# Performance work log

Measured on AMD Instinct MI355X. Metric: run time of the kernel, lower is better.

Reference implementation:

```python
import jax, jax.numpy as jnp
import numpy as np
from jax import lax

NC = 8  # num_classes
NUM_ITERS = 2


def _resize_bilinear_ac(x, out_h, out_w):
    """Bilinear resize with align_corners=True, x: (N, C, H, W)."""
    N, C, H, W = x.shape

    def coords(n_out, n_in):
        if n_out == 1:
            return jnp.zeros((1,), jnp.float32)
        return jnp.linspace(0.0, float(n_in - 1), n_out, dtype=jnp.float32)

    ys = coords(out_h, H)
    xs = coords(out_w, W)
    y0 = jnp.floor(ys).astype(jnp.int32)
    y1 = jnp.minimum(y0 + 1, H - 1)
    wy = (ys - y0.astype(jnp.float32)).astype(x.dtype)
    x0 = jnp.floor(xs).astype(jnp.int32)
    x1 = jnp.minimum(x0 + 1, W - 1)
    wx = (xs - x0.astype(jnp.float32)).astype(x.dtype)

    r0 = x[:, :, y0, :]
    r1 = x[:, :, y1, :]
    r = r0 * (1.0 - wy)[None, None, :, None] + r1 * wy[None, None, :, None]
    c0 = r[:, :, :, x0]
    c1 = r[:, :, :, x1]
    return c0 * (1.0 - wx)[None, None, None, :] + c1 * wx[None, None, None, :]


def _conv2d(x, w, groups=1):
    k = w.shape[-1]
    pad = k // 2
    return lax.conv_general_dilated(
        x, w, window_strides=(1, 1), padding=[(pad, pad), (pad, pad)],
        dimension_numbers=('NCHW', 'OIHW', 'NCHW'), feature_group_count=groups)


def _mean_field_update(unary, guidance, spatial_w, bilateral_w, compat_w):
    Q = jax.nn.softmax(unary, axis=1)
    cw = compat_w[:, :, 0, 0]  # (O, I)
    for _ in range(NUM_ITERS):
        spatial_msg = _conv2d(Q, spatial_w, groups=NC)          # depthwise 3x3
        bilateral_in = jnp.concatenate([Q, guidance], axis=1)   # (N, NC+6, H, W)
        bilateral_msg = _conv2d(bilateral_in, bilateral_w)      # 3x3 dense
        message = spatial_msg + bilateral_msg
        message = jnp.einsum('nchw,oc->nohw', message, cw)      # 1x1 compat conv
        Q = jax.nn.softmax(unary - message, axis=1)
    return Q


def setup_inputs() -> dict:
    key = jax.random.key(0)
    ks = jax.random.split(key, 16)
    inp = {
        'logits': jax.random.normal(ks[0], (8, NC, 512, 512), jnp.float32),
        'image': jax.random.uniform(ks[1], (8, 3, 512, 512), jnp.float32),
        'skip0': jax.random.normal(ks[2], (8, 64, 256, 256), jnp.float32),
        'skip1': jax.random.normal(ks[3], (8, 128, 128, 128), jnp.float32),
        'skip2': jax.random.normal(ks[4], (8, 256, 64, 64), jnp.float32),
        'skip3': jax.random.normal(ks[5], (8, 512, 32, 32), jnp.float32),
        'spatial_w': jax.random.normal(ks[6], (NC, 1, 3, 3), jnp.float32) * 0.1,
        'bilateral_w': jax.random.normal(ks[7], (NC, NC + 6, 3, 3), jnp.float32) * 0.1,
        # compat_conv is initialized to -I (zeros then -= eye) in the module
        'compat_w': (-jnp.eye(NC, dtype=jnp.float32)).reshape(NC, NC, 1, 1),
        'skip_w0': jax.random.normal(ks[8], (3, 64, 1, 1), jnp.float32) * 0.05,
        'skip_b0': jnp.zeros((3,), jnp.float32),
        'skip_w1': jax.random.normal(ks[9], (3, 128, 1, 1), jnp.float32) * 0.05,
        'skip_b1': jnp.zeros((3,), jnp.float32),
        'skip_w2': jax.random.normal(ks[10], (3, 256, 1, 1), jnp.float32) * 0.05,
        'skip_b2': jnp.zeros((3,), jnp.float32),
        'skip_w3': jax.random.normal(ks[11], (3, 512, 1, 1), jnp.float32) * 0.05,
        'skip_b3': jnp.zeros((3,), jnp.float32),
    }
    return inp


def reference(logits, image, skip0, skip1, skip2, skip3,
              spatial_w, bilateral_w, compat_w,
              skip_w0, skip_b0, skip_w1, skip_b1,
              skip_w2, skip_b2, skip_w3, skip_b3):
    H, W = logits.shape[2], logits.shape[3]

    # fuse_skip_features: 1x1 project each skip to 3ch, upsample, average
    skips = [skip0, skip1, skip2, skip3]
    ws = [skip_w0, skip_w1, skip_w2, skip_w3]
    bs = [skip_b0, skip_b1, skip_b2, skip_b3]
    fused = jnp.zeros((logits.shape[0], 3, H, W), logits.dtype)
    for feat, w, b in zip(skips, ws, bs):
        p = jnp.einsum('nchw,oc->nohw', feat, w[:, :, 0, 0]) + b[None, :, None, None]
        fused = fused + _resize_bilinear_ac(p, H, W)
    fused = fused / len(skips)

    guidance = jnp.concatenate([image, fused], axis=1)  # (N, 6, H, W)

    Q_full = _mean_field_update(logits, guidance, spatial_w, bilateral_w, compat_w)

    logits_down = _resize_bilinear_ac(logits, H // 2, W // 2)
    guidance_down = _resize_bilinear_ac(guidance, H // 2, W // 2)
    Q_down = _mean_field_update(logits_down, guidance_down, spatial_w, bilateral_w, compat_w)
    Q_down_up = _resize_bilinear_ac(Q_down, H, W)

    return (Q_full + Q_down_up) / 2.0
```

## Files before the change

### kernel.cpp

```cpp
#include <hip/hip_runtime.h>
#include <hip/hip_fp16.h>
#include <math.h>

#define NB 8
#define NCLS 8
#define NGU 6
#define NBI 14
#define HF 512
#define WF 512
#define HH 256
#define WH 256

#define TOX 32
#define TOY 16
#define SX 36
#define SY 20
#define SPX (SY * SX)
#define R1W 36
#define R1N (18 * 36)
#define R1T 41
#define R2T 32
#define PLANE (SPX * 8)
#define PSTR (PLANE + 32)
#define TILEH (16 + PSTR + PLANE + 16)

typedef _Float16 f16x8 __attribute__((ext_vector_type(8)));
typedef float f32x4 __attribute__((ext_vector_type(4)));

static __device__ __forceinline__ void ac_prep(int o, float scale, int insz,
                                               int& i0, int& i1, float& f) {
    float s = (float)o * scale;
    int ii = (int)floorf(s);
    if (ii > insz - 1) ii = insz - 1;
    if (ii < 0) ii = 0;
    i0 = ii;
    i1 = (ii + 1 < insz) ? (ii + 1) : (insz - 1);
    f = s - (float)ii;
}

static __device__ __forceinline__ void dma16(const _Float16* g, _Float16* l) {
    __builtin_amdgcn_global_load_lds(
        (const __attribute__((address_space(1))) void*)g,
        (__attribute__((address_space(3))) void*)l, 16, 0, 0);
}
static __device__ __forceinline__ void dma16f(const float* g, float* l) {
    __builtin_amdgcn_global_load_lds(
        (const __attribute__((address_space(1))) void*)g,
        (__attribute__((address_space(3))) void*)l, 16, 0, 0);
}

__global__ void k_prep_wf(const float* __restrict__ wsp, const float* __restrict__ wbil,
                          const float* __restrict__ cw, _Float16* __restrict__ wf) {
    __shared__ float sW2[NBI * 72];
    int tid = threadIdx.x;
    if (tid < NBI * 72) {
        int o = tid & 7;
        int t = (tid >> 3) % 9;
        int ci = tid / 72;
        float s = 0.f;
        for (int c = 0; c < NCLS; ++c)
            s += cw[o * NCLS + c] * wbil[((size_t)c * NBI + ci) * 9 + t];
        if (ci < NCLS) s += cw[o * NCLS + ci] * wsp[ci * 9 + t];
        sW2[tid] = s;
    }
    __syncthreads();
    if (tid < 5 * 64) {
        int l = tid & 63;
        int col = l & 15, kg = l >> 4;
        #pragma unroll
        for (int e = 0; e < 8; ++e) {
            int k = (tid >> 6) * 32 + kg * 8 + e;
            int tap = k >> 4, ci = k & 15;
            float v = (tap < 9 && ci < 14 && col < 8) ? sW2[ci * 72 + tap * 8 + col] : 0.f;
            wf[tid * 8 + e] = (_Float16)v;
        }
    }
}

template <int C, int HW>
static __device__ __forceinline__ void skip_run16(
    const float* __restrict__ feat, const float* __restrict__ wg,
    const float* __restrict__ bg, float* __restrict__ out, int idx,
    float* st, float* sw, int tid, int lane, int wv) {
    for (int i = tid; i < 3 * C; i += 256) sw[i] = wg[i];
    const int pxg = idx * 256;
    const int n = pxg / HW;
    const int hw0 = pxg - n * HW;
    const float* fb = feat + (size_t)n * C * HW + hw0;
    float a0 = 0.f, a1 = 0.f, a2 = 0.f;
    for (int g = 0; g < C; g += 16) {
        #pragma unroll
        for (int r = 0; r < 4; ++r)
            dma16f(fb + (size_t)(g + wv + 4 * r) * HW + lane * 4,
                   st + (wv + 4 * r) * 256);
        __syncthreads();
        #pragma unroll
        for (int c = 0; c < 16; ++c) {
            const float v = st[c * 256 + tid];
            a0 = fmaf(sw[g + c], v, a0);
            a1 = fmaf(sw[C + g + c], v, a1);
            a2 = fmaf(sw[2 * C + g + c], v, a2);
        }
        __syncthreads();
    }
    float* op = out + (size_t)n * 3 * HW + hw0 + tid;
    op[0] = bg[0] + a0;
    op[HW] = bg[1] + a1;
    op[2 * (size_t)HW] = bg[2] + a2;
}

__global__ __launch_bounds__(256) void k_skip_all(
    const float* __restrict__ s0, const float* __restrict__ s1,
    const float* __restrict__ s2, const float* __restrict__ s3,
    const float* __restrict__ w0, const float* __restrict__ w1,
    const float* __restrict__ w2, const float* __restrict__ w3,
    const float* __restrict__ b0, const float* __restrict__ b1,
    const float* __restrict__ b2, const float* __restrict__ b3,
    float* __restrict__ p0, float* __restrict__ p1,
    float* __restrict__ p2, float* __restrict__ p3) {
    __shared__ __align__(16) float st[16 * 256];
    __shared__ float sw[3 * 512];
    const int bid = blockIdx.x;
    const int tid = threadIdx.x;
    const int lane = tid & 63;
    const int wv = tid >> 6;
    if (bid < 32)
        skip_run16<512, 1024>(s3, w3, b3, p3, bid, st, sw, tid, lane, wv);
    else if (bid < 160)
        skip_run16<256, 4096>(s2, w2, b2, p2, bid - 32, st, sw, tid, lane, wv);
    else if (bid < 672)
        skip_run16<128, 16384>(s1, w1, b1, p1, bid - 160, st, sw, tid, lane, wv);
    else
        skip_run16<64, 65536>(s0, w0, b0, p0, bid - 672, st, sw, tid, lane, wv);
}

__global__ void k_prep_full(const float* __restrict__ logits, const float* __restrict__ image,
                            const float* __restrict__ p0, const float* __restrict__ p1,
                            const float* __restrict__ p2, const float* __restrict__ p3,
                            _Float16* __restrict__ Gh, _Float16* __restrict__ Q0h) {
    const int HW = HF * WF;
    int t = blockIdx.x * blockDim.x + threadIdx.x;
    if (t >= NB * HW / 2) return;
    int idx = t * 2;
    int n = idx / HW, r = idx - n * HW;
    int y = r / WF, x = r - y * WF;

    const float* ps[4] = {p0, p1, p2, p3};
    const int ss[4] = {256, 128, 64, 32};
    float f[2][3] = {{0.f, 0.f, 0.f}, {0.f, 0.f, 0.f}};
    #pragma unroll
    for (int l = 0; l < 4; ++l) {
        int s = ss[l];
        float scale = (float)(s - 1) / 511.0f;
        int y0, y1;
        float fy;
        ac_prep(y, scale, s, y0, y1, fy);
        const float* pb = ps[l] + (size_t)n * 3 * s * s;
        #pragma unroll
        for (int k = 0; k < 2; ++k) {
            int x0, x1;
            float fx;
            ac_prep(x + k, scale, s, x0, x1, fx);
            #pragma unroll
            for (int o = 0; o < 3; ++o) {
                const float* pp = pb + (size_t)o * s * s;
                float v00 = pp[y0 * s + x0], v01 = pp[y0 * s + x1];
                float v10 = pp[y1 * s + x0], v11 = pp[y1 * s + x1];
                float r0 = v00 * (1.f - fy) + v10 * fy;
                float r1 = v01 * (1.f - fy) + v11 * fy;
                f[k][o] += r0 * (1.f - fx) + r1 * fx;
            }
        }
    }
    const float* ip = image + (size_t)n * 3 * HW + r;
    float2 img[3];
    #pragma unroll
    for (int o = 0; o < 3; ++o) img[o] = *reinterpret_cast<const float2*>(&ip[(size_t)o * HW]);
    const float* up = logits + (size_t)n * NCLS * HW + r;
    float2 u[8];
    #pragma unroll
    for (int o = 0; o < 8; ++o) u[o] = *reinterpret_cast<const float2*>(&up[(size_t)o * HW]);

    f16x8 gv[2], qv[2];
    #pragma unroll
    for (int k = 0; k < 2; ++k) {
        gv[k][0] = (_Float16)(k ? img[0].y : img[0].x);
        gv[k][1] = (_Float16)(k ? img[1].y : img[1].x);
        gv[k][2] = (_Float16)(k ? img[2].y : img[2].x);
        gv[k][3] = (_Float16)(f[k][0] * 0.25f);
        gv[k][4] = (_Float16)(f[k][1] * 0.25f);
        gv[k][5] = (_Float16)(f[k][2] * 0.25f);
        gv[k][6] = (_Float16)0.f;
        gv[k][7] = (_Float16)0.f;
        float e[8];
        float s = 0.f;
        #pragma unroll
        for (int o = 0; o < 8; ++o) { e[o] = __expf(k ? u[o].y : u[o].x); s += e[o]; }
        float inv = 1.f / s;
        #pragma unroll
        for (int o = 0; o < 8; ++o) qv[k][o] = (_Float16)(e[o] * inv);
    }
    *(f16x8*)(Gh + (size_t)idx * 8) = gv[0];
    *(f16x8*)(Gh + (size_t)idx * 8 + 8) = gv[1];
    *(f16x8*)(Q0h + (size_t)idx * 8) = qv[0];
    *(f16x8*)(Q0h + (size_t)idx * 8 + 8) = qv[1];
}

template <bool DOWN, bool UPFOLD>
__global__ __launch_bounds__(256, 4) void k_mf_mfma(
    const float* __restrict__ unary, const _Float16* __restrict__ Q0h,
    const _Float16* __restrict__ Gh, const _Float16* __restrict__ Qd,
    void* __restrict__ QoutV, const _Float16* __restrict__ wfragG,
    int H, int W, int Hs, int Ws) {
    __shared__ __align__(16) _Float16 s_t[TILEH];
    __shared__ __align__(16) _Float16 s_msg[R1N * 8];
    _Float16* tb0 = s_t + 16;
    _Float16* tb1 = s_t + 16 + PSTR;

    const int tid = threadIdx.x;
    const int lane = tid & 63;
    const int wv = tid >> 6;
    const int n = blockIdx.z;
    const int gx0 = blockIdx.x * TOX;
    const int gy0 = blockIdx.y * TOY;
    const int HW = H * W;
    const int HWs = Hs * Ws;

    f16x8 wf[5];
    #pragma unroll
    for (int j = 0; j < 5; ++j)
        wf[j] = *(const f16x8*)(wfragG + (j * 64 + lane) * 8);

    if (tid < 16) s_t[tid] = (_Float16)0.f;
    else if (tid < 48) s_t[5760 + tid] = (_Float16)0.f;
    else if (tid < 64) s_t[11520 + tid] = (_Float16)0.f;

    const bool interior = !DOWN && gx0 >= 2 && (gx0 + TOX + 2) <= W &&
                          gy0 >= 2 && (gy0 + TOY + 2) <= H;

    if (!DOWN && interior) {
        const size_t nb = (size_t)n * HW;
        for (int c = wv; c < 12; c += 4) {
            int px = c * 64 + lane;
            int yy = px / SX, xx = px - yy * SX;
            size_t goff = (nb + (size_t)(gy0 + yy - 2) * W + (gx0 + xx - 2)) * 8;
            if (px < SPX) {
                dma16(Q0h + goff, tb0 + (size_t)c * 64 * 8);
                dma16(Gh + goff, tb1 + (size_t)c * 64 * 8);
            }
        }
    } else {
        const float syc = DOWN ? (float)(Hs - 1) / (float)(H - 1) : 1.f;
        const float sxc = DOWN ? (float)(Ws - 1) / (float)(W - 1) : 1.f;
        for (int i = tid; i < SPX; i += 256) {
            int yy = i / SX, xx = i - yy * SX;
            int gy = gy0 + yy - 2, gx = gx0 + xx - 2;
            f16x8 qv, gv;
            #pragma unroll
            for (int o = 0; o < 8; ++o) { qv[o] = (_Float16)0.f; gv[o] = (_Float16)0.f; }
            if ((unsigned)gy < (unsigned)H && (unsigned)gx < (unsigned)W) {
                if (DOWN) {
                    int y0, y1, x0, x1;
                    float fy, fx;
                    ac_prep(gy, syc, Hs, y0, y1, fy);
                    ac_prep(gx, sxc, Ws, x0, x1, fx);
                    const float w00 = (1.f - fy) * (1.f - fx), w01 = (1.f - fy) * fx;
                    const float w10 = fy * (1.f - fx), w11 = fy * fx;
                    const size_t o00 = (size_t)y0 * Ws + x0, o01 = (size_t)y0 * Ws + x1;
                    const size_t o10 = (size_t)y1 * Ws + x0, o11 = (size_t)y1 * Ws + x1;
                    const float* ubase = unary + (size_t)n * NCLS * HWs;
                    float e[8];
                    float s = 0.f;
                    #pragma unroll
                    for (int o = 0; o < 8; ++o) {
                        const float* up = ubase + (size_t)o * HWs;
                        float u = w00 * up[o00] + w01 * up[o01] + w10 * up[o10] + w11 * up[o11];
                        e[o] = __expf(u);
                        s += e[o];
                    }
                    float inv = 1.f / s;
                    #pragma unroll
                    for (int o = 0; o < 8; ++o) qv[o] = (_Float16)(e[o] * inv);
                    const size_t gb = (size_t)n * HWs;
                    f16x8 ga = *(const f16x8*)(Gh + (gb + o00) * 8);
                    f16x8 gb2 = *(const f16x8*)(Gh + (gb + o01) * 8);
                    f16x8 gc = *(const f16x8*)(Gh + (gb + o10) * 8);
                    f16x8 gd = *(const f16x8*)(Gh + (gb + o11) * 8);
                    #pragma unroll
                    for (int c = 0; c < 8; ++c) {
                        float g = w00 * (float)ga[c] + w01 * (float)gb2[c] +
                                  w10 * (float)gc[c] + w11 * (float)gd[c];
                        gv[c] = (_Float16)g;
                    }
                } else {
                    const size_t off = ((size_t)n * HW + (size_t)gy * W + gx) * 8;
                    qv = *(const f16x8*)(Q0h + off);
                    gv = *(const f16x8*)(Gh + off);
                }
            }
            *(f16x8*)(tb0 + i * 8) = qv;
            *(f16x8*)(tb1 + i * 8) = gv;
        }
    }
    __syncthreads();

    for (int t = wv; t < R1T; t += 4) {
        int pb = t * 16;
        int p = pb + (lane & 15);
        if (p > R1N - 1) p = R1N - 1;
        int qy = p / R1W;
        int yy = 1 + qy, xx = p - qy * R1W;
        int kg = lane >> 4;
        f32x4 acc = {0.f, 0.f, 0.f, 0.f};
        #pragma unroll
        for (int j = 0; j < 5; ++j) {
            int tap = 2 * j + (kg >> 1);
            if (tap > 8) tap = 8;
            int dy = tap / 3 - 1, dx = tap - (tap / 3) * 3 - 1;
            int idx = (yy + dy) * SX + (xx + dx);
            f16x8 af = *(const f16x8*)(tb0 + (kg & 1) * PSTR + idx * 8);
            acc = __builtin_amdgcn_mfma_f32_16x16x32_f16(af, wf[j], acc, 0, 0, 0);
        }
        int ch = lane & 15;
        if (ch < 8) {
            int pxb = pb + (lane >> 4) * 4;
            #pragma unroll
            for (int r = 0; r < 4; ++r) {
                int px = pxb + r;
                if (px < R1N) s_msg[px * 8 + ch] = (_Float16)acc[r];
            }
        }
    }
    __syncthreads();

    for (int i = tid; i < R1N; i += 256) {
        int qy = i / R1W;
        int yy = 1 + qy, xx = i - qy * R1W;
        int gy = gy0 + yy - 2, gx = gx0 + xx - 2;
        if (interior || ((unsigned)gy < (unsigned)H && (unsigned)gx < (unsigned)W)) {
            f16x8 m = *(const f16x8*)(s_msg + i * 8);
            f16x8 q0 = *(const f16x8*)(tb0 + (i + SX) * 8);
            float e[8];
            float s = 0.f;
            #pragma unroll
            for (int o = 0; o < 8; ++o) {
                e[o] = (float)q0[o] * __expf(-(float)m[o]);
                s += e[o];
            }
            float inv = 1.f / s;
            f16x8 q1;
            #pragma unroll
            for (int o = 0; o < 8; ++o) q1[o] = (_Float16)(e[o] * inv);
            *(f16x8*)(tb0 + (i + SX) * 8) = q1;
        }
    }
    f16x8 m1r[2];
    #pragma unroll
    for (int u2 = 0; u2 < 2; ++u2) {
        int i = tid + 256 * u2;
        int oy = i >> 5, ox = i & 31;
        int r1 = (1 + oy) * R1W + (2 + ox);
        m1r[u2] = *(const f16x8*)(s_msg + r1 * 8);
    }
    __syncthreads();

    for (int t = wv; t < R2T; t += 4) {
        int pb = t * 16;
        int p = pb + (lane & 15);
        int yy = 2 + (p >> 5), xx = 2 + (p & 31);
        int kg = lane >> 4;
        f32x4 acc = {0.f, 0.f, 0.f, 0.f};
        #pragma unroll
        for (int j = 0; j < 5; ++j) {
            int tap = 2 * j + (kg >> 1);
            if (tap > 8) tap = 8;
            int dy = tap / 3 - 1, dx = tap - (tap / 3) * 3 - 1;
            int idx = (yy + dy) * SX + (xx + dx);
            f16x8 af = *(const f16x8*)(tb0 + (kg & 1) * PSTR + idx * 8);
            acc = __builtin_amdgcn_mfma_f32_16x16x32_f16(af, wf[j], acc, 0, 0, 0);
        }
        int ch = lane & 15;
        if (ch < 8) {
            int pxb = pb + (lane >> 4) * 4;
            #pragma unroll
            for (int r = 0; r < 4; ++r) s_msg[(pxb + r) * 8 + ch] = (_Float16)acc[r];
        }
    }
    __syncthreads();

    #pragma unroll
    for (int u2 = 0; u2 < 2; ++u2) {
        int i = tid + 256 * u2;
        int oy = i >> 5, ox = i & 31;
        int gy = gy0 + oy, gx = gx0 + ox;
        f16x8 m2 = *(const f16x8*)(s_msg + i * 8);
        f16x8 q1 = *(const f16x8*)(tb0 + ((2 + oy) * SX + (2 + ox)) * 8);
        float e[8];
        float s = 0.f;
        #pragma unroll
        for (int o = 0; o < 8; ++o) {
            e[o] = (float)q1[o] * __expf((float)m1r[u2][o] - (float)m2[o]);
            s += e[o];
        }
        float inv = 1.f / s;
        if (UPFOLD) {
            float* qp = (float*)QoutV + (size_t)n * NCLS * HW + (size_t)gy * W + gx;
            int y0, y1, x0, x1;
            float fy, fx;
            ac_prep(gy, 255.f / 511.f, HH, y0, y1, fy);
            ac_prep(gx, 255.f / 511.f, WH, x0, x1, fx);
            const float w00 = (1.f - fy) * (1.f - fx), w01 = (1.f - fy) * fx;
            const float w10 = fy * (1.f - fx), w11 = fy * fx;
            const size_t qb = (size_t)n * (HH * WH);
            f16x8 qa = *(const f16x8*)(Qd + (qb + (size_t)y0 * WH + x0) * 8);
            f16x8 qbv = *(const f16x8*)(Qd + (qb + (size_t)y0 * WH + x1) * 8);
            f16x8 qc = *(const f16x8*)(Qd + (qb + (size_t)y1 * WH + x0) * 8);
            f16x8 qdv = *(const f16x8*)(Qd + (qb + (size_t)y1 * WH + x1) * 8);
            #pragma unroll
            for (int o = 0; o < 8; ++o) {
                float v = w00 * (float)qa[o] + w01 * (float)qbv[o] +
                          w10 * (float)qc[o] + w11 * (float)qdv[o];
                qp[(size_t)o * HW] = fmaf(0.5f, e[o] * inv, 0.5f * v);
            }
        } else {
            _Float16* qo = (_Float16*)QoutV + ((size_t)n * HW + (size_t)gy * W + gx) * 8;
            f16x8 q2;
            #pragma unroll
            for (int o = 0; o < 8; ++o) q2[o] = (_Float16)(e[o] * inv);
            *(f16x8*)qo = q2;
        }
    }
}

static inline int cdiv(int a, int b) { return (a + b - 1) / b; }

extern "C" void kernel_launch(void* const* d_in, const int* in_sizes, int n_in,
                              void* d_out, int out_size, void* d_ws, size_t ws_size,
                              hipStream_t stream) {
    const float* logits = (const float*)d_in[0];
    const float* image = (const float*)d_in[1];
    const float* skip0 = (const float*)d_in[2];
    const float* skip1 = (const float*)d_in[3];
    const float* skip2 = (const float*)d_in[4];
    const float* skip3 = (const float*)d_in[5];
    const float* spatial_w = (const float*)d_in[6];
    const float* bilateral_w = (const float*)d_in[7];
    const float* compat_w = (const float*)d_in[8];
    const float* skip_w0 = (const float*)d_in[9];
    const float* skip_b0 = (const float*)d_in[10];
    const float* skip_w1 = (const float*)d_in[11];
    const float* skip_b1 = (const float*)d_in[12];
    const float* skip_w2 = (const float*)d_in[13];
    const float* skip_b2 = (const float*)d_in[14];
    const float* skip_w3 = (const float*)d_in[15];
    const float* skip_b3 = (const float*)d_in[16];
    float* out = (float*)d_out;
    float* ws = (float*)d_ws;

    float* p0 = ws + 0;
    float* p1 = ws + 1572864;
    float* p2 = ws + 1966080;
    float* p3 = ws + 2064384;
    _Float16* wfrag = (_Float16*)(ws + 2110000);
    _Float16* Q0h = (_Float16*)(ws + 4194304);
    _Float16* Gh = (_Float16*)(ws + 12582912);
    _Float16* Qdh = (_Float16*)(ws + 20971520);

    const int HWf = HF * WF;

    k_prep_wf<<<1, 1024, 0, stream>>>(spatial_w, bilateral_w, compat_w, wfrag);

    k_skip_all<<<2720, 256, 0, stream>>>(skip0, skip1, skip2, skip3,
                                         skip_w0, skip_w1, skip_w2, skip_w3,
                                         skip_b0, skip_b1, skip_b2, skip_b3,
                                         p0, p1, p2, p3);

    k_prep_full<<<cdiv(NB * HWf / 2, 256), 256, 0, stream>>>(
        logits, image, p0, p1, p2, p3, Gh, Q0h);

    {
        dim3 grid(WH / TOX, HH / TOY, NB);
        k_mf_mfma<true, false><<<grid, 256, 0, stream>>>(
            logits, nullptr, Gh, nullptr, (void*)Qdh, wfrag, HH, WH, HF, WF);
    }

    {
        dim3 grid(WF / TOX, HF / TOY, NB);
        k_mf_mfma<false, true><<<grid, 256, 0, stream>>>(
            nullptr, Q0h, Gh, Qdh, (void*)out, wfrag, HF, WF, HF, WF);
    }
}
```

Measured before the change: 205.9 us.

## Split skip-projection channels across threads with register loads and LDS reduction

Replaces the per-block serial channel loop, which staged 16 channels at a time into LDS via async DMA, with a kernel where each thread loads 8 channels of 4 pixels directly into registers as vector loads. Partial sums over channel slices are then reduced in shared memory. This raises the grid from 2720 to 7680 blocks to expose more memory-level parallelism on a bandwidth-bound projection over roughly 200 MB of skip features. In exchange it adds a tree reduction with several barriers and leaves most threads idle during the final store.

```diff
diff --git a/kernel.cpp b/kernel.cpp
--- a/kernel.cpp
+++ b/kernel.cpp
@@ -39,11 +39,6 @@
 }
 
 static __device__ __forceinline__ void dma16(const _Float16* g, _Float16* l) {
-    __builtin_amdgcn_global_load_lds(
-        (const __attribute__((address_space(1))) void*)g,
-        (__attribute__((address_space(3))) void*)l, 16, 0, 0);
-}
-static __device__ __forceinline__ void dma16f(const float* g, float* l) {
     __builtin_amdgcn_global_load_lds(
         (const __attribute__((address_space(1))) void*)g,
         (__attribute__((address_space(3))) void*)l, 16, 0, 0);
@@ -77,36 +72,56 @@
     }
 }
 
-template <int C, int HW>
-static __device__ __forceinline__ void skip_run16(
+template <int C, int HW, int SLICES, int PXG>
+static __device__ __forceinline__ void skip_gemm(
     const float* __restrict__ feat, const float* __restrict__ wg,
-    const float* __restrict__ bg, float* __restrict__ out, int idx,
-    float* st, float* sw, int tid, int lane, int wv) {
+    const float* __restrict__ bg, float* __restrict__ out, int bidl,
+    float* sw, f32x4* sred, int tid) {
     for (int i = tid; i < 3 * C; i += 256) sw[i] = wg[i];
-    const int pxg = idx * 256;
-    const int n = pxg / HW;
-    const int hw0 = pxg - n * HW;
-    const float* fb = feat + (size_t)n * C * HW + hw0;
-    float a0 = 0.f, a1 = 0.f, a2 = 0.f;
-    for (int g = 0; g < C; g += 16) {
-        #pragma unroll
-        for (int r = 0; r < 4; ++r)
-            dma16f(fb + (size_t)(g + wv + 4 * r) * HW + lane * 4,
-                   st + (wv + 4 * r) * 256);
+    __syncthreads();
+    const int slice = tid / PXG;
+    const int pxg = tid - slice * PXG;
+    const int pxbase = bidl * (PXG * 4);
+    const int n = pxbase / HW;
+    const int hw0 = pxbase - n * HW;
+    const float* fp = feat + ((size_t)n * C + slice * 8) * HW + hw0 + pxg * 4;
+
+    f32x4 v[8];
+    #pragma unroll
+    for (int j = 0; j < 8; ++j)
+        v[j] = *reinterpret_cast<const f32x4*>(fp + (size_t)j * HW);
+
+    f32x4 a0 = {0.f, 0.f, 0.f, 0.f};
+    f32x4 a1 = {0.f, 0.f, 0.f, 0.f};
+    f32x4 a2 = {0.f, 0.f, 0.f, 0.f};
+    #pragma unroll
+    for (int j = 0; j < 8; ++j) {
+        const int c = slice * 8 + j;
+        a0 += v[j] * sw[c];
+        a1 += v[j] * sw[C + c];
+        a2 += v[j] * sw[2 * C + c];
+    }
+    sred[0 * 256 + tid] = a0;
+    sred[1 * 256 + tid] = a1;
+    sred[2 * 256 + tid] = a2;
+    __syncthreads();
+    for (int s = 128; s > PXG; s >>= 1) {
+        if (tid < s) {
+            sred[tid] += sred[tid + s];
+            sred[256 + tid] += sred[256 + tid + s];
+            sred[512 + tid] += sred[512 + tid + s];
+        }
         __syncthreads();
-        #pragma unroll
-        for (int c = 0; c < 16; ++c) {
-            const float v = st[c * 256 + tid];
-            a0 = fmaf(sw[g + c], v, a0);
-            a1 = fmaf(sw[C + g + c], v, a1);
-            a2 = fmaf(sw[2 * C + g + c], v, a2);
-        }
-        __syncthreads();
-    }
-    float* op = out + (size_t)n * 3 * HW + hw0 + tid;
-    op[0] = bg[0] + a0;
-    op[HW] = bg[1] + a1;
-    op[2 * (size_t)HW] = bg[2] + a2;
+    }
+    if (tid < PXG) {
+        float* op = out + (size_t)n * 3 * HW + hw0 + tid * 4;
+        f32x4 r0 = sred[tid] + sred[tid + PXG] + bg[0];
+        f32x4 r1 = sred[256 + tid] + sred[256 + tid + PXG] + bg[1];
+        f32x4 r2 = sred[512 + tid] + sred[512 + tid + PXG] + bg[2];
+        *reinterpret_cast<f32x4*>(op) = r0;
+        *reinterpret_cast<f32x4*>(op + HW) = r1;
+        *reinterpret_cast<f32x4*>(op + 2 * (size_t)HW) = r2;
+    }
 }
 
 __global__ __launch_bounds__(256) void k_skip_all(
@@ -118,20 +133,18 @@
     const float* __restrict__ b2, const float* __restrict__ b3,
     float* __restrict__ p0, float* __restrict__ p1,
     float* __restrict__ p2, float* __restrict__ p3) {
-    __shared__ __align__(16) float st[16 * 256];
+    __shared__ __align__(16) f32x4 sred[3 * 256];
     __shared__ float sw[3 * 512];
     const int bid = blockIdx.x;
     const int tid = threadIdx.x;
-    const int lane = tid & 63;
-    const int wv = tid >> 6;
-    if (bid < 32)
-        skip_run16<512, 1024>(s3, w3, b3, p3, bid, st, sw, tid, lane, wv);
-    else if (bid < 160)
-        skip_run16<256, 4096>(s2, w2, b2, p2, bid - 32, st, sw, tid, lane, wv);
-    else if (bid < 672)
-        skip_run16<128, 16384>(s1, w1, b1, p1, bid - 160, st, sw, tid, lane, wv);
+    if (bid < 4096)
+        skip_gemm<64, 65536, 8, 32>(s0, w0, b0, p0, bid, sw, sred, tid);
+    else if (bid < 6144)
+        skip_gemm<128, 16384, 16, 16>(s1, w1, b1, p1, bid - 4096, sw, sred, tid);
+    else if (bid < 7168)
+        skip_gemm<256, 4096, 32, 8>(s2, w2, b2, p2, bid - 6144, sw, sred, tid);
     else
-        skip_run16<64, 65536>(s0, w0, b0, p0, bid - 672, st, sw, tid, lane, wv);
+        skip_gemm<512, 1024, 64, 4>(s3, w3, b3, p3, bid - 7168, sw, sred, tid);
 }
 
 __global__ void k_prep_full(const float* __restrict__ logits, const float* __restrict__ image,
@@ -470,7 +483,7 @@
 
     k_prep_wf<<<1, 1024, 0, stream>>>(spatial_w, bilateral_w, compat_w, wfrag);
 
-    k_skip_all<<<2720, 256, 0, stream>>>(skip0, skip1, skip2, skip3,
+    k_skip_all<<<7680, 256, 0, stream>>>(skip0, skip1, skip2, skip3,
                                          skip_w0, skip_w1, skip_w2, skip_w3,
                                          skip_b0, skip_b1, skip_b2, skip_b3,
                                          p0, p1, p2, p3);
```

After: 190.5 us (median of 2 runs). 1.08x faster.
